# Kernel optimization log

Hardware: AMD Instinct MI355X
Metric: run time of the kernel (lower is better)

## Reference

```python
import jax, jax.numpy as jnp
import numpy as np

N = 20000        # nodes
E = 160000       # directed edges (self-loops added in reference, as PyG GATConv does)
IN = 128         # in_channels
OUT = 128        # out_channels
H = 36           # heads of conv1 (head kwarg)
C = 36           # per-head channels of conv1 (== head kwarg)
HID = H * C      # 1296, conv1 concat output
NEG_SLOPE = 0.2  # PyG GATConv default


def gat_layer(x, src, dst, W, a_src, a_dst, bias, heads, ch, concat, num_nodes):
    """One PyG-style GATConv (eval mode, self-loops already in src/dst)."""
    h = (x @ W).reshape(num_nodes, heads, ch)               # [N,H,C]
    alpha_s = jnp.sum(h * a_src, axis=-1)                   # [N,H]
    alpha_d = jnp.sum(h * a_dst, axis=-1)                   # [N,H]
    e = jax.nn.leaky_relu(alpha_s[src] + alpha_d[dst], NEG_SLOPE)  # [E,H]
    # segment softmax over incoming edges of each target node
    m = jax.ops.segment_max(e, dst, num_segments=num_nodes)        # [N,H]
    m = jnp.where(jnp.isfinite(m), m, 0.0)                  # nodes with no in-edges
    ex = jnp.exp(e - m[dst])                                # [E,H]
    denom = jax.ops.segment_sum(ex, dst, num_segments=num_nodes)   # [N,H]
    alpha = ex / (denom[dst] + 1e-16)                       # [E,H]
    # weighted scatter-aggregate of source features
    out = jax.ops.segment_sum(h[src] * alpha[:, :, None], dst, num_segments=num_nodes)  # [N,H,C]
    out = out.reshape(num_nodes, heads * ch) if concat else out.mean(axis=1)
    return out + bias


def setup_inputs() -> dict:
    key = jax.random.key(0)
    ks = jax.random.split(key, 12)
    x = jax.random.normal(ks[0], (N, IN), jnp.float32)
    edge_index = jax.random.randint(ks[1], (2, E), 0, N, dtype=jnp.int64)
    # conv1 params: heads=36, out per head=36, concat
    W1 = jax.random.normal(ks[2], (IN, H * C), jnp.float32) / np.float32(np.sqrt(IN))
    a_src1 = jax.random.normal(ks[3], (H, C), jnp.float32) * 0.1
    a_dst1 = jax.random.normal(ks[4], (H, C), jnp.float32) * 0.1
    b1 = jnp.zeros((HID,), jnp.float32)
    # conv2 params: heads=1, out=OUT, no concat
    W2 = jax.random.normal(ks[5], (HID, OUT), jnp.float32) / np.float32(np.sqrt(HID))
    a_src2 = jax.random.normal(ks[6], (1, OUT), jnp.float32) * 0.1
    a_dst2 = jax.random.normal(ks[7], (1, OUT), jnp.float32) * 0.1
    b2 = jnp.zeros((OUT,), jnp.float32)
    return {"x": x, "edge_index": edge_index,
            "W1": W1, "a_src1": a_src1, "a_dst1": a_dst1, "b1": b1,
            "W2": W2, "a_src2": a_src2, "a_dst2": a_dst2, "b2": b2}


def reference(x, edge_index, W1, a_src1, a_dst1, b1, W2, a_src2, a_dst2, b2):
    num_nodes = x.shape[0]
    loop = jnp.arange(num_nodes, dtype=edge_index.dtype)
    src = jnp.concatenate([edge_index[0], loop])   # add self-loops (PyG default)
    dst = jnp.concatenate([edge_index[1], loop])
    h = jax.nn.relu(gat_layer(x, src, dst, W1, a_src1, a_dst1, b1,
                              heads=H, ch=C, concat=True, num_nodes=num_nodes))
    out = jax.nn.relu(gat_layer(h, src, dst, W2, a_src2, a_dst2, b2,
                                heads=1, ch=OUT, concat=False, num_nodes=num_nodes))
    return out
```

## Files before the change

### kernel.cpp

```cpp
#include <hip/hip_runtime.h>

#define N_NODES 20000
#define E_EDGES 160000
#define ET (E_EDGES + N_NODES)
#define IN_CH 128
#define HID 1296
#define HEADS 36
#define CPH 36
#define OUT_CH 128
#define KP2 1344
#define NEG_SLOPE 0.2f

typedef __attribute__((ext_vector_type(8))) short bf16x8;
typedef __attribute__((ext_vector_type(8))) unsigned short ushort8;
typedef __attribute__((ext_vector_type(4))) float floatx4;

__device__ __forceinline__ float bf2f(unsigned short u) {
    union { unsigned int i; float f; } c; c.i = ((unsigned int)u) << 16; return c.f;
}
__device__ __forceinline__ unsigned short f2bf(float f) {
    union { float f; unsigned int i; } c; c.f = f;
    unsigned int r = c.i + 0x7FFF + ((c.i >> 16) & 1);
    return (unsigned short)(r >> 16);
}
__device__ __forceinline__ float lrelu(float v) {
    return (v > 0.f) ? v : NEG_SLOPE * v;
}

#define NX (N_NODES * IN_CH / 4)
#define NW1 (HID * IN_CH)
#define NW2 (OUT_CH * KP2)
#define NPREP (NX + NW1 + NW2)
__global__ __launch_bounds__(256) void k_prepcnt(const float* __restrict__ x,
                                                 unsigned short* __restrict__ xb,
                                                 const float* __restrict__ W1,
                                                 unsigned short* __restrict__ W1T,
                                                 const float* __restrict__ W2,
                                                 unsigned short* __restrict__ W2T,
                                                 const int* __restrict__ ei,
                                                 int* __restrict__ cnt) {
    int gid = blockIdx.x * 256 + threadIdx.x;
    if (gid < NX) {
        float4 v = ((const float4*)x)[gid];
        ushort4 o; o.x = f2bf(v.x); o.y = f2bf(v.y); o.z = f2bf(v.z); o.w = f2bf(v.w);
        ((ushort4*)xb)[gid] = o;
    } else if (gid < NX + NW1) {
        int g = gid - NX;
        int n = g >> 7, k = g & 127;
        W1T[g] = f2bf(W1[(size_t)k * HID + n]);
    } else if (gid < NPREP) {
        int g = gid - NX - NW1;
        int n = g / KP2, k = g - n * KP2;
        W2T[g] = (k < HID) ? f2bf(W2[(size_t)k * OUT_CH + n]) : 0;
    } else if (gid < NPREP + ET) {
        int e = gid - NPREP;
        int d = (e < E_EDGES) ? ei[E_EDGES + e] : (e - E_EDGES);
        atomicAdd(&cnt[d], 1);
    }
}

__global__ __launch_bounds__(256) void k_gemm1(const unsigned short* __restrict__ xb,
                                               const unsigned short* __restrict__ W1T,
                                               unsigned short* __restrict__ h1b) {
    __shared__ unsigned short As[128][136];
    __shared__ unsigned short Bs[64][136];
    int tid = threadIdx.x;
    int r0 = blockIdx.x * 128;
    int n0 = blockIdx.y * 64;
#pragma unroll
    for (int i = 0; i < 8; i++) {
        int c = tid + i * 256;
        int row = c >> 4, kc = (c & 15) * 8;
        int gr = min(r0 + row, N_NODES - 1);
        *(bf16x8*)&As[row][kc] = *(const bf16x8*)(xb + (size_t)gr * IN_CH + kc);
    }
#pragma unroll
    for (int i = 0; i < 4; i++) {
        int c = tid + i * 256;
        int row = c >> 4, kc = (c & 15) * 8;
        int gn = min(n0 + row, HID - 1);
        *(bf16x8*)&Bs[row][kc] = *(const bf16x8*)(W1T + (size_t)gn * IN_CH + kc);
    }
    __syncthreads();
    int lane = tid & 63, w = tid >> 6;
    int quad = lane >> 4, l15 = lane & 15;
    int mbase = w * 32;
    floatx4 acc[2][4];
#pragma unroll
    for (int i = 0; i < 2; i++)
#pragma unroll
        for (int j = 0; j < 4; j++) acc[i][j] = (floatx4){0.f, 0.f, 0.f, 0.f};
#pragma unroll
    for (int kc = 0; kc < 128; kc += 32) {
        bf16x8 a0 = *(const bf16x8*)&As[mbase + l15][kc + quad * 8];
        bf16x8 a1 = *(const bf16x8*)&As[mbase + 16 + l15][kc + quad * 8];
#pragma unroll
        for (int j = 0; j < 4; j++) {
            bf16x8 b = *(const bf16x8*)&Bs[j * 16 + l15][kc + quad * 8];
            acc[0][j] = __builtin_amdgcn_mfma_f32_16x16x32_bf16(a0, b, acc[0][j], 0, 0, 0);
            acc[1][j] = __builtin_amdgcn_mfma_f32_16x16x32_bf16(a1, b, acc[1][j], 0, 0, 0);
        }
    }
#pragma unroll
    for (int i = 0; i < 2; i++)
#pragma unroll
        for (int j = 0; j < 4; j++) {
            int colc = n0 + j * 16 + l15;
            if (colc >= HID) continue;
#pragma unroll
            for (int r = 0; r < 4; r++) {
                int row = r0 + mbase + i * 16 + quad * 4 + r;
                if (row < N_NODES)
                    h1b[(size_t)row * HID + colc] = f2bf(acc[i][j][r]);
            }
        }
}

__global__ __launch_bounds__(256) void k_gemm2(const unsigned short* __restrict__ A,
                                               const unsigned short* __restrict__ W2T,
                                               float* __restrict__ h2a,
                                               float* __restrict__ h2b) {
    __shared__ unsigned short As[32][40];
    __shared__ unsigned short Bs[128][40];
    int tid = threadIdx.x;
    int r0 = blockIdx.x * 32;
    int kbase = blockIdx.y * 672;
    int lane = tid & 63, w = tid >> 6;
    int quad = lane >> 4, l15 = lane & 15;
    int nbase = w * 32;
    floatx4 acc[2][2];
#pragma unroll
    for (int i = 0; i < 2; i++)
#pragma unroll
        for (int j = 0; j < 2; j++) acc[i][j] = (floatx4){0.f, 0.f, 0.f, 0.f};

    for (int it = 0; it < 21; it++) {
        int k0 = kbase + it * 32;
        __syncthreads();
        if (tid < 128) {
            int row = tid >> 2, kc = (tid & 3) * 8;
            *(bf16x8*)&As[row][kc] = *(const bf16x8*)(A + (size_t)(r0 + row) * KP2 + k0 + kc);
        }
#pragma unroll
        for (int i = 0; i < 2; i++) {
            int c = tid + i * 256;
            int row = c >> 2, kc = (c & 3) * 8;
            *(bf16x8*)&Bs[row][kc] = *(const bf16x8*)(W2T + (size_t)row * KP2 + k0 + kc);
        }
        __syncthreads();
        bf16x8 a0 = *(const bf16x8*)&As[l15][quad * 8];
        bf16x8 a1 = *(const bf16x8*)&As[16 + l15][quad * 8];
        bf16x8 b0 = *(const bf16x8*)&Bs[nbase + l15][quad * 8];
        bf16x8 b1 = *(const bf16x8*)&Bs[nbase + 16 + l15][quad * 8];
        acc[0][0] = __builtin_amdgcn_mfma_f32_16x16x32_bf16(a0, b0, acc[0][0], 0, 0, 0);
        acc[1][0] = __builtin_amdgcn_mfma_f32_16x16x32_bf16(a1, b0, acc[1][0], 0, 0, 0);
        acc[0][1] = __builtin_amdgcn_mfma_f32_16x16x32_bf16(a0, b1, acc[0][1], 0, 0, 0);
        acc[1][1] = __builtin_amdgcn_mfma_f32_16x16x32_bf16(a1, b1, acc[1][1], 0, 0, 0);
    }
    float* dst = (blockIdx.y == 0) ? h2a : h2b;
#pragma unroll
    for (int i = 0; i < 2; i++)
#pragma unroll
        for (int j = 0; j < 2; j++) {
            int colc = nbase + j * 16 + l15;
#pragma unroll
            for (int r = 0; r < 4; r++) {
                int row = r0 + i * 16 + quad * 4 + r;
                dst[(size_t)row * OUT_CH + colc] = acc[i][j][r];
            }
        }
}

__global__ __launch_bounds__(256) void k_alpha1(const unsigned short* __restrict__ h1b,
                                                const float* __restrict__ a_src,
                                                const float* __restrict__ a_dst,
                                                float* __restrict__ as,
                                                float* __restrict__ ad) {
    __shared__ float s_a[HEADS * CPH], s_b[HEADS * CPH];
    int tid = threadIdx.x;
    for (int i = tid; i < HEADS * CPH; i += 256) { s_a[i] = a_src[i]; s_b[i] = a_dst[i]; }
    __syncthreads();
    int gid = blockIdx.x * 256 + tid;
    if (gid >= N_NODES * HEADS) return;
    int n = gid / HEADS, h = gid - n * HEADS;
    const unsigned short* row = h1b + (size_t)n * HID + h * CPH;
    float ss = 0.f, sd = 0.f;
#pragma unroll
    for (int c = 0; c < CPH; c += 2) {
        uint u = *(const uint*)(row + c);
        float v0 = bf2f((unsigned short)(u & 0xFFFF));
        float v1 = bf2f((unsigned short)(u >> 16));
        ss += v0 * s_a[h * CPH + c] + v1 * s_a[h * CPH + c + 1];
        sd += v0 * s_b[h * CPH + c] + v1 * s_b[h * CPH + c + 1];
    }
    as[gid] = ss;
    ad[gid] = sd;
}

__global__ __launch_bounds__(1024) void k_scan(const int* __restrict__ cnt, int* __restrict__ rowp) {
    __shared__ int sh[1024];
    const int PER = 20;
    int t = threadIdx.x;
    int base = t * PER;
    int local[PER];
    int sum = 0;
    for (int i = 0; i < PER; i++) {
        int idx = base + i;
        int v = (idx < N_NODES) ? cnt[idx] : 0;
        local[i] = sum;
        sum += v;
    }
    sh[t] = sum;
    __syncthreads();
    for (int off = 1; off < 1024; off <<= 1) {
        int v = (t >= off) ? sh[t - off] : 0;
        __syncthreads();
        sh[t] += v;
        __syncthreads();
    }
    int offset = (t == 0) ? 0 : sh[t - 1];
    for (int i = 0; i < PER; i++) {
        int idx = base + i;
        if (idx < N_NODES) rowp[idx] = offset + local[i];
    }
    if (t == 1023) rowp[N_NODES] = sh[1023];
}

__global__ void k_fill(const int* __restrict__ ei, const int* __restrict__ rowp,
                       int* __restrict__ cursor, int* __restrict__ col) {
    int e = blockIdx.x * 256 + threadIdx.x;
    if (e >= ET) return;
    int s, d;
    if (e < E_EDGES) { s = ei[e]; d = ei[E_EDGES + e]; }
    else { s = e - E_EDGES; d = s; }
    int pos = rowp[d] + atomicAdd(&cursor[d], 1);
    col[pos] = s;
}

__global__ __launch_bounds__(192) void k_agg1(const unsigned short* __restrict__ h1b,
                                              const float* __restrict__ as1,
                                              const float* __restrict__ ad1,
                                              const int* __restrict__ rowp,
                                              const int* __restrict__ col,
                                              const float* __restrict__ b1,
                                              unsigned short* __restrict__ out1b) {
    int n = blockIdx.x;
    int tid = threadIdx.x;
    int r0 = rowp[n], r1 = rowp[n + 1];
    const bool act = tid < 162;
    int c0 = tid * 8;
    int h0 = act ? c0 / 36 : 0;
    int h7 = act ? (c0 + 7) / 36 : 0;
    int split = (h0 + 1) * 36 - c0;
    float sel[8];
#pragma unroll
    for (int j = 0; j < 8; j++) sel[j] = (j < split) ? 0.f : 1.f;
    float ad0 = 0.f, ad7 = 0.f;
    if (act) {
        ad0 = ad1[(size_t)n * HEADS + h0];
        ad7 = (h7 == h0) ? ad0 : ad1[(size_t)n * HEADS + h7];
    }
    float acc[8];
#pragma unroll
    for (int j = 0; j < 8; j++) acc[j] = 0.f;
    float sA = 0.f, sB = 0.f;

    if (act) {
        int e = r0;
        for (; e + 4 <= r1; e += 4) {
            int s0 = col[e], s1 = col[e + 1], s2 = col[e + 2], s3 = col[e + 3];
            float wA0 = __expf(lrelu(as1[(size_t)s0 * HEADS + h0] + ad0));
            float wB0 = __expf(lrelu(as1[(size_t)s0 * HEADS + h7] + ad7));
            float wA1 = __expf(lrelu(as1[(size_t)s1 * HEADS + h0] + ad0));
            float wB1 = __expf(lrelu(as1[(size_t)s1 * HEADS + h7] + ad7));
            float wA2 = __expf(lrelu(as1[(size_t)s2 * HEADS + h0] + ad0));
            float wB2 = __expf(lrelu(as1[(size_t)s2 * HEADS + h7] + ad7));
            float wA3 = __expf(lrelu(as1[(size_t)s3 * HEADS + h0] + ad0));
            float wB3 = __expf(lrelu(as1[(size_t)s3 * HEADS + h7] + ad7));
            ushort8 v0 = *(const ushort8*)(h1b + (size_t)s0 * HID + c0);
            ushort8 v1 = *(const ushort8*)(h1b + (size_t)s1 * HID + c0);
            ushort8 v2 = *(const ushort8*)(h1b + (size_t)s2 * HID + c0);
            ushort8 v3 = *(const ushort8*)(h1b + (size_t)s3 * HID + c0);
            sA += wA0 + wA1 + wA2 + wA3;
            sB += wB0 + wB1 + wB2 + wB3;
            float dw0 = wB0 - wA0, dw1 = wB1 - wA1, dw2 = wB2 - wA2, dw3 = wB3 - wA3;
#pragma unroll
            for (int j = 0; j < 8; j++) {
                acc[j] = fmaf(fmaf(sel[j], dw0, wA0), bf2f(v0[j]), acc[j]);
                acc[j] = fmaf(fmaf(sel[j], dw1, wA1), bf2f(v1[j]), acc[j]);
                acc[j] = fmaf(fmaf(sel[j], dw2, wA2), bf2f(v2[j]), acc[j]);
                acc[j] = fmaf(fmaf(sel[j], dw3, wA3), bf2f(v3[j]), acc[j]);
            }
        }
        for (; e < r1; e++) {
            int s = col[e];
            float wA = __expf(lrelu(as1[(size_t)s * HEADS + h0] + ad0));
            float wB = __expf(lrelu(as1[(size_t)s * HEADS + h7] + ad7));
            ushort8 vv = *(const ushort8*)(h1b + (size_t)s * HID + c0);
            sA += wA; sB += wB;
            float dw = wB - wA;
#pragma unroll
            for (int j = 0; j < 8; j++)
                acc[j] = fmaf(fmaf(sel[j], dw, wA), bf2f(vv[j]), acc[j]);
        }
    }
    if (tid < KP2 / 8) {
        ushort8 o;
        if (act) {
            float invA = 1.f / (sA + 1e-16f);
            float invB = 1.f / (sB + 1e-16f);
            float dinv = invB - invA;
#pragma unroll
            for (int j = 0; j < 8; j++) {
                float vv = acc[j] * fmaf(sel[j], dinv, invA) + b1[c0 + j];
                o[j] = f2bf(fmaxf(vv, 0.f));
            }
        } else {
#pragma unroll
            for (int j = 0; j < 8; j++) o[j] = 0;
        }
        *(ushort8*)(out1b + (size_t)n * KP2 + c0) = o;
    }
}

__global__ __launch_bounds__(64) void k_alpha2c(const float* __restrict__ h2a,
                                                const float* __restrict__ h2b,
                                                unsigned short* __restrict__ h2q,
                                                const float* __restrict__ a_src,
                                                const float* __restrict__ a_dst,
                                                float* __restrict__ as,
                                                float* __restrict__ ad) {
    int n = blockIdx.x;
    int t = threadIdx.x;
    size_t base = (size_t)n * OUT_CH;
    float v0 = h2a[base + t] + h2b[base + t];
    float v1 = h2a[base + t + 64] + h2b[base + t + 64];
    h2q[base + t] = f2bf(v0);
    h2q[base + t + 64] = f2bf(v1);
    float ss = v0 * a_src[t] + v1 * a_src[t + 64];
    float sd = v0 * a_dst[t] + v1 * a_dst[t + 64];
    for (int off = 32; off > 0; off >>= 1) {
        ss += __shfl_down(ss, off);
        sd += __shfl_down(sd, off);
    }
    if (t == 0) { as[n] = ss; ad[n] = sd; }
}

__global__ __launch_bounds__(64) void k_agg2(const unsigned short* __restrict__ h2q,
                                             const float* __restrict__ as,
                                             const float* __restrict__ ad,
                                             const int* __restrict__ rowp,
                                             const int* __restrict__ col,
                                             const float* __restrict__ b2,
                                             float* __restrict__ out) {
    int n = blockIdx.x;
    int t = threadIdx.x;
    int r0 = rowp[n], r1 = rowp[n + 1];
    float adn = ad[n];
    __shared__ float wsh[32];
    __shared__ int csh[32];
    float acc0 = 0.f, acc1 = 0.f;
    float sw = 0.f;
    for (int p0 = r0; p0 < r1; p0 += 32) {
        int ne = min(32, r1 - p0);
        __syncthreads();
        if (t < ne) {
            int s = col[p0 + t];
            csh[t] = s;
            wsh[t] = __expf(lrelu(as[s] + adn));
        }
        __syncthreads();
        int e = 0;
        for (; e + 4 <= ne; e += 4) {
            uint u0 = *(const uint*)(h2q + (size_t)csh[e + 0] * OUT_CH + t * 2);
            uint u1 = *(const uint*)(h2q + (size_t)csh[e + 1] * OUT_CH + t * 2);
            uint u2 = *(const uint*)(h2q + (size_t)csh[e + 2] * OUT_CH + t * 2);
            uint u3 = *(const uint*)(h2q + (size_t)csh[e + 3] * OUT_CH + t * 2);
            float w0 = wsh[e], w1 = wsh[e + 1], w2 = wsh[e + 2], w3 = wsh[e + 3];
            sw += w0 + w1 + w2 + w3;
            acc0 += w0 * bf2f((unsigned short)(u0 & 0xFFFF)) + w1 * bf2f((unsigned short)(u1 & 0xFFFF))
                  + w2 * bf2f((unsigned short)(u2 & 0xFFFF)) + w3 * bf2f((unsigned short)(u3 & 0xFFFF));
            acc1 += w0 * bf2f((unsigned short)(u0 >> 16)) + w1 * bf2f((unsigned short)(u1 >> 16))
                  + w2 * bf2f((unsigned short)(u2 >> 16)) + w3 * bf2f((unsigned short)(u3 >> 16));
        }
        for (; e < ne; e++) {
            uint ua = *(const uint*)(h2q + (size_t)csh[e] * OUT_CH + t * 2);
            float wa = wsh[e];
            sw += wa;
            acc0 += wa * bf2f((unsigned short)(ua & 0xFFFF));
            acc1 += wa * bf2f((unsigned short)(ua >> 16));
        }
    }
    float inv = 1.f / (sw + 1e-16f);
    float o0 = acc0 * inv + b2[t * 2];
    float o1 = acc1 * inv + b2[t * 2 + 1];
    out[(size_t)n * OUT_CH + t * 2]     = (o0 > 0.f) ? o0 : 0.f;
    out[(size_t)n * OUT_CH + t * 2 + 1] = (o1 > 0.f) ? o1 : 0.f;
}

extern "C" void kernel_launch(void* const* d_in, const int* in_sizes, int n_in,
                              void* d_out, int out_size, void* d_ws, size_t ws_size,
                              hipStream_t stream) {
    const float* x      = (const float*)d_in[0];
    const int*   ei     = (const int*)d_in[1];
    const float* W1     = (const float*)d_in[2];
    const float* a_src1 = (const float*)d_in[3];
    const float* a_dst1 = (const float*)d_in[4];
    const float* b1     = (const float*)d_in[5];
    const float* W2     = (const float*)d_in[6];
    const float* a_src2 = (const float*)d_in[7];
    const float* a_dst2 = (const float*)d_in[8];
    const float* b2     = (const float*)d_in[9];
    float* out = (float*)d_out;

    unsigned short* h1b   = (unsigned short*)d_ws;
    unsigned short* out1b = h1b + (size_t)N_NODES * HID;
    unsigned short* xb    = out1b + (size_t)N_NODES * KP2;
    unsigned short* W1T   = xb + (size_t)N_NODES * IN_CH;
    unsigned short* W2T   = W1T + (size_t)HID * IN_CH;
    float* fbase = (float*)(W2T + NW2);
    float* as1  = fbase;
    float* ad1  = as1 + (size_t)N_NODES * HEADS;
    float* h2a  = ad1 + (size_t)N_NODES * HEADS;
    float* h2b  = h2a + (size_t)N_NODES * OUT_CH;
    unsigned short* h2q = (unsigned short*)(h2b + (size_t)N_NODES * OUT_CH);
    float* as2  = (float*)(h2q + (size_t)N_NODES * OUT_CH);
    float* ad2  = as2 + N_NODES;
    int* cnt    = (int*)(ad2 + N_NODES);
    int* cursor = cnt + N_NODES;
    int* rowp   = cursor + N_NODES;
    int* colx   = rowp + (N_NODES + 1);

    hipMemsetAsync(cnt, 0, (size_t)(2 * N_NODES) * sizeof(int), stream);

    k_prepcnt<<<(NPREP + ET + 255) / 256, 256, 0, stream>>>(x, xb, W1, W1T, W2, W2T, ei, cnt);
    k_scan<<<1, 1024, 0, stream>>>(cnt, rowp);
    k_fill<<<(ET + 255) / 256, 256, 0, stream>>>(ei, rowp, cursor, colx);
    k_gemm1<<<dim3(157, 21), 256, 0, stream>>>(xb, W1T, h1b);
    k_alpha1<<<(N_NODES * HEADS + 255) / 256, 256, 0, stream>>>(h1b, a_src1, a_dst1, as1, ad1);
    k_agg1<<<N_NODES, 192, 0, stream>>>(h1b, as1, ad1, rowp, colx, b1, out1b);
    k_gemm2<<<dim3(625, 2), 256, 0, stream>>>(out1b, W2T, h2a, h2b);
    k_alpha2c<<<N_NODES, 64, 0, stream>>>(h2a, h2b, h2q, a_src2, a_dst2, as2, ad2);
    k_agg2<<<N_NODES, 64, 0, stream>>>(h2q, as2, ad2, rowp, colx, b2, out);
}
```

Measured before the change: 275.6 us.

## Fuse split-K reduction and layer-2 attention scores into gemm2 epilogue

The gemm2 kernel now runs both K halves inside one 512-thread block and reduces the two partial tiles in shared memory. Its epilogue also writes the bf16 features and the per-node source and destination attention scores, so the separate k_alpha2c kernel goes away. This drops one launch and the fp32 round trip of two N×128 partial buffers through global memory. The cost is more shared memory per block and fewer blocks (625 instead of 1250), which may reduce latency hiding.

```diff
diff --git a/kernel.cpp b/kernel.cpp
--- a/kernel.cpp
+++ b/kernel.cpp
@@ -116,18 +116,25 @@
         }
 }
 
-__global__ __launch_bounds__(256) void k_gemm2(const unsigned short* __restrict__ A,
+__global__ __launch_bounds__(512) void k_gemm2(const unsigned short* __restrict__ A,
                                                const unsigned short* __restrict__ W2T,
-                                               float* __restrict__ h2a,
-                                               float* __restrict__ h2b) {
-    __shared__ unsigned short As[32][40];
-    __shared__ unsigned short Bs[128][40];
+                                               const float* __restrict__ a_src2,
+                                               const float* __restrict__ a_dst2,
+                                               unsigned short* __restrict__ h2q,
+                                               float* __restrict__ as2,
+                                               float* __restrict__ ad2) {
+    __shared__ unsigned short As[2][32][40];
+    __shared__ unsigned short Bs[2][128][40];
+    __shared__ float Cs[32][132];
     int tid = threadIdx.x;
     int r0 = blockIdx.x * 32;
-    int kbase = blockIdx.y * 672;
-    int lane = tid & 63, w = tid >> 6;
+    int khalf = tid >> 8;
+    int tl = tid & 255;
+    int lane = tid & 63;
+    int wl = (tid >> 6) & 3;
     int quad = lane >> 4, l15 = lane & 15;
-    int nbase = w * 32;
+    int nbase = wl * 32;
+    int kbase = khalf * 672;
     floatx4 acc[2][2];
 #pragma unroll
     for (int i = 0; i < 2; i++)
@@ -137,38 +144,71 @@
     for (int it = 0; it < 21; it++) {
         int k0 = kbase + it * 32;
         __syncthreads();
-        if (tid < 128) {
-            int row = tid >> 2, kc = (tid & 3) * 8;
-            *(bf16x8*)&As[row][kc] = *(const bf16x8*)(A + (size_t)(r0 + row) * KP2 + k0 + kc);
+        if (tl < 128) {
+            int row = tl >> 2, kc = (tl & 3) * 8;
+            *(bf16x8*)&As[khalf][row][kc] = *(const bf16x8*)(A + (size_t)(r0 + row) * KP2 + k0 + kc);
         }
 #pragma unroll
         for (int i = 0; i < 2; i++) {
-            int c = tid + i * 256;
+            int c = tl + i * 256;
             int row = c >> 2, kc = (c & 3) * 8;
-            *(bf16x8*)&Bs[row][kc] = *(const bf16x8*)(W2T + (size_t)row * KP2 + k0 + kc);
-        }
-        __syncthreads();
-        bf16x8 a0 = *(const bf16x8*)&As[l15][quad * 8];
-        bf16x8 a1 = *(const bf16x8*)&As[16 + l15][quad * 8];
-        bf16x8 b0 = *(const bf16x8*)&Bs[nbase + l15][quad * 8];
-        bf16x8 b1 = *(const bf16x8*)&Bs[nbase + 16 + l15][quad * 8];
+            *(bf16x8*)&Bs[khalf][row][kc] = *(const bf16x8*)(W2T + (size_t)row * KP2 + k0 + kc);
+        }
+        __syncthreads();
+        bf16x8 a0 = *(const bf16x8*)&As[khalf][l15][quad * 8];
+        bf16x8 a1 = *(const bf16x8*)&As[khalf][16 + l15][quad * 8];
+        bf16x8 b0 = *(const bf16x8*)&Bs[khalf][nbase + l15][quad * 8];
+        bf16x8 b1 = *(const bf16x8*)&Bs[khalf][nbase + 16 + l15][quad * 8];
         acc[0][0] = __builtin_amdgcn_mfma_f32_16x16x32_bf16(a0, b0, acc[0][0], 0, 0, 0);
         acc[1][0] = __builtin_amdgcn_mfma_f32_16x16x32_bf16(a1, b0, acc[1][0], 0, 0, 0);
         acc[0][1] = __builtin_amdgcn_mfma_f32_16x16x32_bf16(a0, b1, acc[0][1], 0, 0, 0);
         acc[1][1] = __builtin_amdgcn_mfma_f32_16x16x32_bf16(a1, b1, acc[1][1], 0, 0, 0);
     }
-    float* dst = (blockIdx.y == 0) ? h2a : h2b;
-#pragma unroll
-    for (int i = 0; i < 2; i++)
-#pragma unroll
-        for (int j = 0; j < 2; j++) {
-            int colc = nbase + j * 16 + l15;
-#pragma unroll
-            for (int r = 0; r < 4; r++) {
-                int row = r0 + i * 16 + quad * 4 + r;
-                dst[(size_t)row * OUT_CH + colc] = acc[i][j][r];
-            }
-        }
+    __syncthreads();
+    if (khalf == 0) {
+#pragma unroll
+        for (int i = 0; i < 2; i++)
+#pragma unroll
+            for (int j = 0; j < 2; j++)
+#pragma unroll
+                for (int r = 0; r < 4; r++)
+                    Cs[i * 16 + quad * 4 + r][nbase + j * 16 + l15] = acc[i][j][r];
+    }
+    __syncthreads();
+    if (khalf == 1) {
+#pragma unroll
+        for (int i = 0; i < 2; i++)
+#pragma unroll
+            for (int j = 0; j < 2; j++)
+#pragma unroll
+                for (int r = 0; r < 4; r++)
+                    Cs[i * 16 + quad * 4 + r][nbase + j * 16 + l15] += acc[i][j][r];
+    }
+    __syncthreads();
+    {
+        int row = tid >> 4;
+        int c8 = (tid & 15) * 8;
+        float v[8];
+        ushort8 o;
+        float ss = 0.f, sd = 0.f;
+#pragma unroll
+        for (int j = 0; j < 8; j++) {
+            v[j] = Cs[row][c8 + j];
+            o[j] = f2bf(v[j]);
+            ss = fmaf(v[j], a_src2[c8 + j], ss);
+            sd = fmaf(v[j], a_dst2[c8 + j], sd);
+        }
+        *(ushort8*)(h2q + (size_t)(r0 + row) * OUT_CH + c8) = o;
+#pragma unroll
+        for (int off = 8; off > 0; off >>= 1) {
+            ss += __shfl_down(ss, off);
+            sd += __shfl_down(sd, off);
+        }
+        if ((tid & 15) == 0) {
+            as2[r0 + row] = ss;
+            ad2[r0 + row] = sd;
+        }
+    }
 }
 
 __global__ __launch_bounds__(256) void k_alpha1(const unsigned short* __restrict__ h1b,
@@ -323,29 +363,6 @@
     }
 }
 
-__global__ __launch_bounds__(64) void k_alpha2c(const float* __restrict__ h2a,
-                                                const float* __restrict__ h2b,
-                                                unsigned short* __restrict__ h2q,
-                                                const float* __restrict__ a_src,
-                                                const float* __restrict__ a_dst,
-                                                float* __restrict__ as,
-                                                float* __restrict__ ad) {
-    int n = blockIdx.x;
-    int t = threadIdx.x;
-    size_t base = (size_t)n * OUT_CH;
-    float v0 = h2a[base + t] + h2b[base + t];
-    float v1 = h2a[base + t + 64] + h2b[base + t + 64];
-    h2q[base + t] = f2bf(v0);
-    h2q[base + t + 64] = f2bf(v1);
-    float ss = v0 * a_src[t] + v1 * a_src[t + 64];
-    float sd = v0 * a_dst[t] + v1 * a_dst[t + 64];
-    for (int off = 32; off > 0; off >>= 1) {
-        ss += __shfl_down(ss, off);
-        sd += __shfl_down(sd, off);
-    }
-    if (t == 0) { as[n] = ss; ad[n] = sd; }
-}
-
 __global__ __launch_bounds__(64) void k_agg2(const unsigned short* __restrict__ h2q,
                                              const float* __restrict__ as,
                                              const float* __restrict__ ad,
@@ -421,9 +438,7 @@
     float* fbase = (float*)(W2T + NW2);
     float* as1  = fbase;
     float* ad1  = as1 + (size_t)N_NODES * HEADS;
-    float* h2a  = ad1 + (size_t)N_NODES * HEADS;
-    float* h2b  = h2a + (size_t)N_NODES * OUT_CH;
-    unsigned short* h2q = (unsigned short*)(h2b + (size_t)N_NODES * OUT_CH);
+    unsigned short* h2q = (unsigned short*)(ad1 + (size_t)N_NODES * HEADS);
     float* as2  = (float*)(h2q + (size_t)N_NODES * OUT_CH);
     float* ad2  = as2 + N_NODES;
     int* cnt    = (int*)(ad2 + N_NODES);
@@ -439,7 +454,6 @@
     k_gemm1<<<dim3(157, 21), 256, 0, stream>>>(xb, W1T, h1b);
     k_alpha1<<<(N_NODES * HEADS + 255) / 256, 256, 0, stream>>>(h1b, a_src1, a_dst1, as1, ad1);
     k_agg1<<<N_NODES, 192, 0, stream>>>(h1b, as1, ad1, rowp, colx, b1, out1b);
-    k_gemm2<<<dim3(625, 2), 256, 0, stream>>>(out1b, W2T, h2a, h2b);
-    k_alpha2c<<<N_NODES, 64, 0, stream>>>(h2a, h2b, h2q, a_src2, a_dst2, as2, ad2);
+    k_gemm2<<<625, 512, 0, stream>>>(out1b, W2T, a_src2, a_dst2, h2q, as2, ad2);
     k_agg2<<<N_NODES, 64, 0, stream>>>(h2q, as2, ad2, rowp, colx, b2, out);
 }
```

New measurement: 271.1 us. No clear change (-1.7%).
